# Kernel optimization log

Hardware: AMD Instinct MI355X
Metric: run time of the kernel (lower is better)

Reference implementation:

```python
import jax, jax.numpy as jnp
import numpy as np

B, C, F = 8, 2048, 128


def setup_inputs() -> dict:
    key = jax.random.key(0)
    ks = jax.random.split(key, 13)
    features = jax.random.normal(ks[0], (B, C, F), dtype=jnp.float32)
    # sparse-ish boolean adjacency masks over operations
    pred_mask = jax.random.uniform(ks[1], (B, C, C)) < 0.05
    succ_mask = jax.random.uniform(ks[2], (B, C, C)) < 0.05
    same_type_mask = jax.random.uniform(ks[3], (B, C, C)) < 0.10

    def linear(k, fan_in, fan_out):
        kw, kb = jax.random.split(k)
        bound = 1.0 / np.sqrt(fan_in)
        W = jax.random.uniform(kw, (fan_in, fan_out), minval=-bound, maxval=bound, dtype=jnp.float32)
        b = jax.random.uniform(kb, (fan_out,), minval=-bound, maxval=bound, dtype=jnp.float32)
        return W, b

    W_enc, b_enc = linear(ks[4], F, 4 * F)
    W_space, b_space = linear(ks[5], 3 * F, F)
    W_same, b_same = linear(ks[6], 2 * F, F)
    W_mix, b_mix = linear(ks[7], 2 * F, F)
    return {
        "features": features,
        "pred_mask": pred_mask,
        "succ_mask": succ_mask,
        "same_type_mask": same_type_mask,
        "W_enc": W_enc, "b_enc": b_enc,
        "W_space": W_space, "b_space": b_space,
        "W_same": W_same, "b_same": b_same,
        "W_mix": W_mix, "b_mix": b_mix,
    }


def reference(features, pred_mask, succ_mask, same_type_mask,
              W_enc, b_enc, W_space, b_space, W_same, b_same, W_mix, b_mix):
    # encoder: [B,C,F] -> [B,C,4F], split into origin + 3 message features
    enc = features @ W_enc + b_enc
    origin, e_pred, e_succ, e_same = jnp.split(enc, 4, axis=-1)

    def masked_mean(mask, e):
        # original builds (B,C,C,F) broadcast product then sums over 'other';
        # mathematically this is mask @ e with a clamped-degree divisor.
        m = mask.astype(e.dtype)                         # [B,C,C]
        deg = jnp.maximum(m.sum(-1, keepdims=True), 1.0)  # [B,C,1]
        return jnp.einsum('bij,bjf->bif', m, e) / deg

    pred_f = masked_mean(pred_mask, e_pred)
    succ_f = masked_mean(succ_mask, e_succ)
    same_f = masked_mean(same_type_mask, e_same)

    space_mixed = jnp.concatenate([pred_f, origin, succ_f], axis=-1) @ W_space + b_space
    same_mixed = jnp.concatenate([origin, same_f], axis=-1) @ W_same + b_same
    return jnp.concatenate([space_mixed, same_mixed], axis=-1) @ W_mix + b_mix
```

## Files before the change

### kernel.cpp

```cpp
#include <hip/hip_runtime.h>
#include <stdint.h>

typedef unsigned int uint;
typedef unsigned short ushort;
typedef unsigned char uchar;
typedef __attribute__((ext_vector_type(8))) short bf16x8;
typedef __attribute__((ext_vector_type(4))) float f32x4;

__device__ __forceinline__ ushort f2bf(float f) {
  uint u = __builtin_bit_cast(uint, f);
  return (ushort)((u + 0x7FFFu + ((u >> 16) & 1u)) >> 16);
}

__global__ __launch_bounds__(256) void k_detect(
    const uint* __restrict__ mp, const uint* __restrict__ ms,
    const uint* __restrict__ mt, int* __restrict__ esz) {
  int bid = blockIdx.x;
  const uint* m = (bid < 64) ? mp : (bid < 128) ? ms : mt;
  uint v = m[(size_t)(bid & 63) * 65521 + threadIdx.x];
  if (!(v == 0u || v == 1u || v == 0x3F800000u)) atomicAnd(esz, 0);
}

__global__ __launch_bounds__(256) void k_fuse1(
    const float* __restrict__ Ws, const float* __restrict__ Wsame,
    const float* __restrict__ Wm, float* __restrict__ T1, float* __restrict__ T2) {
  int idx = blockIdx.x * 256 + threadIdx.x;
  if (idx >= 81920) return;
  int r = idx >> 7, n = idx & 127;
  float s = 0.f;
  if (r < 384) {
    for (int c = 0; c < 128; ++c) s += Ws[r * 128 + c] * Wm[c * 128 + n];
    T1[r * 128 + n] = s;
  } else {
    int rr = r - 384;
    for (int c = 0; c < 128; ++c) s += Wsame[rr * 128 + c] * Wm[(128 + c) * 128 + n];
    T2[rr * 128 + n] = s;
  }
}

__global__ __launch_bounds__(256) void k_fuse2(
    const float* __restrict__ We, const float* __restrict__ be,
    const float* __restrict__ bs, const float* __restrict__ bsame,
    const float* __restrict__ bm, const float* __restrict__ Wm,
    const float* __restrict__ T1, const float* __restrict__ T2,
    ushort* __restrict__ UT, float* __restrict__ cvec) {
  int idx = blockIdx.x * 256 + threadIdx.x;
  if (idx < 65536) {
    int y = idx >> 14, n = (idx >> 7) & 127, k = idx & 127;
    float s = 0.f;
    if (y == 0)
      for (int m = 0; m < 128; ++m)
        s += We[k * 512 + m] * (T1[(128 + m) * 128 + n] + T2[m * 128 + n]);
    else if (y == 1)
      for (int m = 0; m < 128; ++m) s += We[k * 512 + 128 + m] * T1[m * 128 + n];
    else if (y == 2)
      for (int m = 0; m < 128; ++m) s += We[k * 512 + 256 + m] * T1[(256 + m) * 128 + n];
    else
      for (int m = 0; m < 128; ++m) s += We[k * 512 + 384 + m] * T2[(128 + m) * 128 + n];
    UT[((size_t)y * 128 + n) * 128 + k] = f2bf(s);
  } else if (idx < 66048) {
    int cid = idx - 65536, cv = cid >> 7, n = cid & 127;
    float s = 0.f;
    if (cv == 0) {
      for (int m = 0; m < 128; ++m)
        s += be[m] * (T1[(128 + m) * 128 + n] + T2[m * 128 + n]);
      for (int c = 0; c < 128; ++c) s += bs[c] * Wm[c * 128 + n];
      for (int c = 0; c < 128; ++c) s += bsame[c] * Wm[(128 + c) * 128 + n];
      s += bm[n];
    } else if (cv == 1) {
      for (int m = 0; m < 128; ++m) s += be[128 + m] * T1[m * 128 + n];
    } else if (cv == 2) {
      for (int m = 0; m < 128; ++m) s += be[256 + m] * T1[(256 + m) * 128 + n];
    } else {
      for (int m = 0; m < 128; ++m) s += be[384 + m] * T2[(128 + m) * 128 + n];
    }
    cvec[cv * 128 + n] = s;
  }
}

__global__ __launch_bounds__(256) void k_enc(
    const float* __restrict__ feat, const ushort* __restrict__ UT,
    const float* __restrict__ cvec, float* __restrict__ out,
    ushort* __restrict__ eT0, ushort* __restrict__ eT1, ushort* __restrict__ eT2) {
  __shared__ ushort As[64 * 72];
  __shared__ ushort Bs[128 * 72];
  __shared__ ushort stage[8192];
  const int t = threadIdx.x;
  const int gm0 = blockIdx.x * 64;
  const int y = blockIdx.y;
  const int lane = t & 63, wave = t >> 6;
  const int m0w = (wave >> 1) * 32, n0w = (wave & 1) * 64;
  const int quad = lane >> 4, lr = lane & 15;
  const int am = t >> 2, aq = t & 3;
  const int bn = t >> 1, bh = t & 1;
  f32x4 acc[2][4] = {};
  for (int k0 = 0; k0 < 128; k0 += 64) {
    const float* asrc = feat + (size_t)(gm0 + am) * 128 + k0 + aq * 16;
    float4 f0 = *(const float4*)asrc;
    float4 f1 = *(const float4*)(asrc + 4);
    float4 f2 = *(const float4*)(asrc + 8);
    float4 f3 = *(const float4*)(asrc + 12);
    ushort h[16];
    h[0] = f2bf(f0.x); h[1] = f2bf(f0.y); h[2] = f2bf(f0.z); h[3] = f2bf(f0.w);
    h[4] = f2bf(f1.x); h[5] = f2bf(f1.y); h[6] = f2bf(f1.z); h[7] = f2bf(f1.w);
    h[8] = f2bf(f2.x); h[9] = f2bf(f2.y); h[10] = f2bf(f2.z); h[11] = f2bf(f2.w);
    h[12] = f2bf(f3.x); h[13] = f2bf(f3.y); h[14] = f2bf(f3.z); h[15] = f2bf(f3.w);
    const ushort* bsrc = UT + ((size_t)y * 128 + bn) * 128 + k0 + bh * 32;
    bf16x8 bv0 = *(const bf16x8*)bsrc;
    bf16x8 bv1 = *(const bf16x8*)(bsrc + 8);
    bf16x8 bv2 = *(const bf16x8*)(bsrc + 16);
    bf16x8 bv3 = *(const bf16x8*)(bsrc + 24);
    *(bf16x8*)&As[am * 72 + aq * 16] = *(bf16x8*)&h[0];
    *(bf16x8*)&As[am * 72 + aq * 16 + 8] = *(bf16x8*)&h[8];
    *(bf16x8*)&Bs[bn * 72 + bh * 32] = bv0;
    *(bf16x8*)&Bs[bn * 72 + bh * 32 + 8] = bv1;
    *(bf16x8*)&Bs[bn * 72 + bh * 32 + 16] = bv2;
    *(bf16x8*)&Bs[bn * 72 + bh * 32 + 24] = bv3;
    __syncthreads();
#pragma unroll
    for (int kc = 0; kc < 2; ++kc) {
      bf16x8 a[2], b[4];
#pragma unroll
      for (int i = 0; i < 2; ++i)
        a[i] = *(const bf16x8*)&As[(m0w + i * 16 + lr) * 72 + kc * 32 + quad * 8];
#pragma unroll
      for (int j = 0; j < 4; ++j)
        b[j] = *(const bf16x8*)&Bs[(n0w + j * 16 + lr) * 72 + kc * 32 + quad * 8];
#pragma unroll
      for (int i = 0; i < 2; ++i)
#pragma unroll
        for (int j = 0; j < 4; ++j)
          acc[i][j] = __builtin_amdgcn_mfma_f32_16x16x32_bf16(a[i], b[j], acc[i][j], 0, 0, 0);
    }
    __syncthreads();
  }
  if (y == 0) {
#pragma unroll
    for (int i = 0; i < 2; ++i)
#pragma unroll
      for (int j = 0; j < 4; ++j)
#pragma unroll
        for (int r = 0; r < 4; ++r) {
          int m = gm0 + m0w + i * 16 + quad * 4 + r;
          int n = n0w + j * 16 + lr;
          out[(size_t)m * 128 + n] = acc[i][j][r] + cvec[n];
        }
  } else {
#pragma unroll
    for (int i = 0; i < 2; ++i)
#pragma unroll
      for (int j = 0; j < 4; ++j)
#pragma unroll
        for (int r = 0; r < 4; ++r) {
          int rl = m0w + i * 16 + quad * 4 + r;
          int n = n0w + j * 16 + lr;
          int kc = rl >> 5, qd = (rl >> 3) & 3, e = rl & 7;
          stage[((((n >> 4) * 2 + kc) * 4 + qd) * 16 + (n & 15)) * 8 + e] =
              f2bf(acc[i][j][r]);
        }
    __syncthreads();
    ushort* eT = (y == 1) ? eT0 : (y == 2) ? eT1 : eT2;
    ushort* dst = eT + ((size_t)(gm0 >> 11) * 32 + ((gm0 >> 6) & 31)) * 8192 + t * 32;
    const ushort* src = stage + t * 32;
#pragma unroll
    for (int p = 0; p < 4; ++p)
      *(bf16x8*)(dst + p * 8) = *(const bf16x8*)(src + p * 8);
  }
}

__global__ __launch_bounds__(256, 3) void k_mm(
    const void* __restrict__ mp, const void* __restrict__ ms,
    const void* __restrict__ mt, const ushort* __restrict__ eT0,
    const ushort* __restrict__ eT1, const ushort* __restrict__ eT2,
    const float* __restrict__ cvec, float* __restrict__ out,
    const int* __restrict__ esz_p) {
  __shared__ uint degs[64];
  const int t = threadIdx.x;
  const int id = blockIdx.x;
  const int xcd = id & 7, q = id >> 3;
  const int mtile = q & 31, gg = xcd * 3 + (q >> 5);
  const int b = gg & 7, mid = gg >> 3;
  const void* mask = (mid == 0) ? mp : (mid == 1) ? ms : mt;
  const ushort* eT = (mid == 0) ? eT0 : (mid == 1) ? eT1 : eT2;
  const float* cm = cvec + (mid + 1) * 128;
  const bool is4 = (*esz_p != 0);
  if (t < 64) degs[t] = 0;
  __syncthreads();

  const int lane = t & 63, wave = t >> 6;
  const int m0w = (wave >> 1) * 32, n0w = (wave & 1) * 64;
  const int quad = lane >> 4, lr = lane & 15;
  const int jb = n0w >> 4;
  const size_t rowbase = (size_t)b * 2048 + mtile * 64;
  const size_t r0 = rowbase + m0w + lr;
  const size_t r1 = r0 + 16;
  const uint* A40 = (const uint*)mask + r0 * 2048 + quad * 8;
  const uint* A41 = (const uint*)mask + r1 * 2048 + quad * 8;
  const uchar* A10 = (const uchar*)mask + r0 * 2048 + quad * 8;
  const uchar* A11 = (const uchar*)mask + r1 * 2048 + quad * 8;
  const ushort* bbase = eT + (size_t)b * 32 * 8192 + quad * 128 + lr * 8;

  f32x4 acc[2][4] = {};
  uint4 pa[2][2][2];
  uint2 pa8[2][2];
  bf16x8 pb[2][4];
  int cnt0 = 0, cnt1 = 0;

#define LOAD_ITER(IT, BUF)                                                   \
  do {                                                                       \
    int it_ = (IT);                                                          \
    if (is4) {                                                               \
      const uint* p0_ = A40 + it_ * 32;                                      \
      const uint* p1_ = A41 + it_ * 32;                                      \
      pa[BUF][0][0] = *(const uint4*)p0_;                                    \
      pa[BUF][0][1] = *(const uint4*)(p0_ + 4);                              \
      pa[BUF][1][0] = *(const uint4*)p1_;                                    \
      pa[BUF][1][1] = *(const uint4*)(p1_ + 4);                              \
    } else {                                                                 \
      pa8[BUF][0] = *(const uint2*)(A10 + it_ * 32);                         \
      pa8[BUF][1] = *(const uint2*)(A11 + it_ * 32);                         \
    }                                                                        \
    const ushort* bp_ = bbase + (it_ >> 1) * 8192 + (it_ & 1) * 512;         \
    _Pragma("unroll")                                                        \
    for (int j_ = 0; j_ < 4; ++j_)                                           \
      pb[BUF][j_] = *(const bf16x8*)(bp_ + (jb + j_) * 1024);                \
  } while (0)

  LOAD_ITER(0, 0);
#pragma unroll 2
  for (int it = 0; it < 64; ++it) {
    const int cur = it & 1;
    if (it < 63) LOAD_ITER(it + 1, cur ^ 1);
    union { bf16x8 v; uint u[4]; } af[2];
    if (is4) {
#pragma unroll
      for (int i = 0; i < 2; ++i) {
        uint x[8] = {pa[cur][i][0].x, pa[cur][i][0].y, pa[cur][i][0].z,
                     pa[cur][i][0].w, pa[cur][i][1].x, pa[cur][i][1].y,
                     pa[cur][i][1].z, pa[cur][i][1].w};
        int c = 0;
#pragma unroll
        for (int p = 0; p < 4; ++p) {
          af[i].u[p] = (x[2 * p] ? 0x3F80u : 0u) | (x[2 * p + 1] ? 0x3F800000u : 0u);
          c += (x[2 * p] != 0u) + (x[2 * p + 1] != 0u);
        }
        if (i == 0) cnt0 += c; else cnt1 += c;
      }
    } else {
#pragma unroll
      for (int i = 0; i < 2; ++i) {
        uint wl = pa8[cur][i].x, wh = pa8[cur][i].y;
        int c = 0;
        af[i].u[0] = ((wl & 0xFFu) ? 0x3F80u : 0u) | ((wl & 0xFF00u) ? 0x3F800000u : 0u);
        af[i].u[1] = ((wl & 0xFF0000u) ? 0x3F80u : 0u) | ((wl & 0xFF000000u) ? 0x3F800000u : 0u);
        af[i].u[2] = ((wh & 0xFFu) ? 0x3F80u : 0u) | ((wh & 0xFF00u) ? 0x3F800000u : 0u);
        af[i].u[3] = ((wh & 0xFF0000u) ? 0x3F80u : 0u) | ((wh & 0xFF000000u) ? 0x3F800000u : 0u);
        c += ((wl & 0xFFu) != 0u) + ((wl & 0xFF00u) != 0u) +
             ((wl & 0xFF0000u) != 0u) + ((wl & 0xFF000000u) != 0u) +
             ((wh & 0xFFu) != 0u) + ((wh & 0xFF00u) != 0u) +
             ((wh & 0xFF0000u) != 0u) + ((wh & 0xFF000000u) != 0u);
        if (i == 0) cnt0 += c; else cnt1 += c;
      }
    }
#pragma unroll
    for (int i = 0; i < 2; ++i)
#pragma unroll
      for (int j = 0; j < 4; ++j)
        acc[i][j] = __builtin_amdgcn_mfma_f32_16x16x32_bf16(af[i].v, pb[cur][j], acc[i][j], 0, 0, 0);
  }
#undef LOAD_ITER

  if ((wave & 1) == 0) {
    atomicAdd(&degs[m0w + lr], (uint)cnt0);
    atomicAdd(&degs[m0w + 16 + lr], (uint)cnt1);
  }
  __syncthreads();

#pragma unroll
  for (int i = 0; i < 2; ++i)
#pragma unroll
    for (int r = 0; r < 4; ++r) {
      int ml = m0w + i * 16 + quad * 4 + r;
      uint d = degs[ml];
      float inv = 1.0f / (float)(d > 0u ? d : 1u);
      float ind = (d > 0u) ? 1.0f : 0.0f;
#pragma unroll
      for (int j = 0; j < 4; ++j) {
        int n = n0w + j * 16 + lr;
        atomicAdd(&out[(rowbase + ml) * 128 + n], acc[i][j][r] * inv + ind * cm[n]);
      }
    }
}

extern "C" void kernel_launch(void* const* d_in, const int* in_sizes, int n_in,
                              void* d_out, int out_size, void* d_ws,
                              size_t ws_size, hipStream_t stream) {
  const float* features = (const float*)d_in[0];
  const void* pred = d_in[1];
  const void* succ = d_in[2];
  const void* same = d_in[3];
  const float* W_enc = (const float*)d_in[4];
  const float* b_enc = (const float*)d_in[5];
  const float* W_space = (const float*)d_in[6];
  const float* b_space = (const float*)d_in[7];
  const float* W_same = (const float*)d_in[8];
  const float* b_same = (const float*)d_in[9];
  const float* W_mix = (const float*)d_in[10];
  const float* b_mix = (const float*)d_in[11];
  float* out = (float*)d_out;

  char* wsb = (char*)d_ws;
  ushort* UT = (ushort*)wsb;
  float* cvec = (float*)(wsb + 131072);
  float* T1 = (float*)(wsb + 133120);
  float* T2 = (float*)(wsb + 329728);
  ushort* eT0 = (ushort*)(wsb + 460800);
  ushort* eT1 = (ushort*)(wsb + 460800 + 4194304);
  ushort* eT2 = (ushort*)(wsb + 460800 + 8388608);
  int* esz = (int*)(wsb + 460800 + 12582912);

  hipMemsetAsync(esz, 1, 4, stream);
  k_detect<<<192, 256, 0, stream>>>((const uint*)pred, (const uint*)succ,
                                    (const uint*)same, esz);
  k_fuse1<<<320, 256, 0, stream>>>(W_space, W_same, W_mix, T1, T2);
  k_fuse2<<<258, 256, 0, stream>>>(W_enc, b_enc, b_space, b_same, b_mix, W_mix,
                                   T1, T2, UT, cvec);
  k_enc<<<dim3(256, 4), 256, 0, stream>>>(features, UT, cvec, out, eT0, eT1, eT2);
  k_mm<<<768, 256, 0, stream>>>(pred, succ, same, eT0, eT1, eT2, cvec, out, esz);
}
```

Measured before the change: 470.3 us.

## Replace output atomics with per-mask partial buffers and a reduction kernel

The mask-matmul kernel now writes its per-mask results into three separate partial buffers instead of atomically adding into the output, and a new kernel sums them into the output. The k-index permutation of the mask and encoded-feature layout is changed so each lane loads contiguous 16-byte mask chunks. The main loop is restructured with explicit two-stage register prefetch for the 4-byte mask path, while the byte-mask path drops prefetching. This removes global float atomics at the cost of extra partial-buffer traffic and one more launch.

```diff
diff --git a/kernel.cpp b/kernel.cpp
--- a/kernel.cpp
+++ b/kernel.cpp
@@ -41,7 +41,7 @@
 __global__ __launch_bounds__(256) void k_fuse2(
     const float* __restrict__ We, const float* __restrict__ be,
     const float* __restrict__ bs, const float* __restrict__ bsame,
-    const float* __restrict__ bm, const float* __restrict__ Wm,
+    const float* __restrict__ bm_, const float* __restrict__ Wm,
     const float* __restrict__ T1, const float* __restrict__ T2,
     ushort* __restrict__ UT, float* __restrict__ cvec) {
   int idx = blockIdx.x * 256 + threadIdx.x;
@@ -66,7 +66,7 @@
         s += be[m] * (T1[(128 + m) * 128 + n] + T2[m * 128 + n]);
       for (int c = 0; c < 128; ++c) s += bs[c] * Wm[c * 128 + n];
       for (int c = 0; c < 128; ++c) s += bsame[c] * Wm[(128 + c) * 128 + n];
-      s += bm[n];
+      s += bm_[n];
     } else if (cv == 1) {
       for (int m = 0; m < 128; ++m) s += be[128 + m] * T1[m * 128 + n];
     } else if (cv == 2) {
@@ -152,9 +152,10 @@
       for (int j = 0; j < 4; ++j)
 #pragma unroll
         for (int r = 0; r < 4; ++r) {
-          int rl = m0w + i * 16 + quad * 4 + r;
+          int cl = m0w + i * 16 + quad * 4 + r;
+          int u = (cl & 32) + (((cl >> 2) & 3) * 8) + ((cl >> 4) & 1) * 4 + (cl & 3);
           int n = n0w + j * 16 + lr;
-          int kc = rl >> 5, qd = (rl >> 3) & 3, e = rl & 7;
+          int kc = u >> 5, qd = (u >> 3) & 3, e = u & 7;
           stage[((((n >> 4) * 2 + kc) * 4 + qd) * 16 + (n & 15)) * 8 + e] =
               f2bf(acc[i][j][r]);
         }
@@ -172,7 +173,8 @@
     const void* __restrict__ mp, const void* __restrict__ ms,
     const void* __restrict__ mt, const ushort* __restrict__ eT0,
     const ushort* __restrict__ eT1, const ushort* __restrict__ eT2,
-    const float* __restrict__ cvec, float* __restrict__ out,
+    const float* __restrict__ cvec, float* __restrict__ P0,
+    float* __restrict__ P1, float* __restrict__ P2,
     const int* __restrict__ esz_p) {
   __shared__ uint degs[64];
   const int t = threadIdx.x;
@@ -182,6 +184,7 @@
   const int b = gg & 7, mid = gg >> 3;
   const void* mask = (mid == 0) ? mp : (mid == 1) ? ms : mt;
   const ushort* eT = (mid == 0) ? eT0 : (mid == 1) ? eT1 : eT2;
+  float* Pm = (mid == 0) ? P0 : (mid == 1) ? P1 : P2;
   const float* cm = cvec + (mid + 1) * 128;
   const bool is4 = (*esz_p != 0);
   if (t < 64) degs[t] = 0;
@@ -194,81 +197,104 @@
   const size_t rowbase = (size_t)b * 2048 + mtile * 64;
   const size_t r0 = rowbase + m0w + lr;
   const size_t r1 = r0 + 16;
-  const uint* A40 = (const uint*)mask + r0 * 2048 + quad * 8;
-  const uint* A41 = (const uint*)mask + r1 * 2048 + quad * 8;
-  const uchar* A10 = (const uchar*)mask + r0 * 2048 + quad * 8;
-  const uchar* A11 = (const uchar*)mask + r1 * 2048 + quad * 8;
   const ushort* bbase = eT + (size_t)b * 32 * 8192 + quad * 128 + lr * 8;
 
   f32x4 acc[2][4] = {};
-  uint4 pa[2][2][2];
-  uint2 pa8[2][2];
-  bf16x8 pb[2][4];
   int cnt0 = 0, cnt1 = 0;
 
-#define LOAD_ITER(IT, BUF)                                                   \
-  do {                                                                       \
-    int it_ = (IT);                                                          \
-    if (is4) {                                                               \
-      const uint* p0_ = A40 + it_ * 32;                                      \
-      const uint* p1_ = A41 + it_ * 32;                                      \
-      pa[BUF][0][0] = *(const uint4*)p0_;                                    \
-      pa[BUF][0][1] = *(const uint4*)(p0_ + 4);                              \
-      pa[BUF][1][0] = *(const uint4*)p1_;                                    \
-      pa[BUF][1][1] = *(const uint4*)(p1_ + 4);                              \
-    } else {                                                                 \
-      pa8[BUF][0] = *(const uint2*)(A10 + it_ * 32);                         \
-      pa8[BUF][1] = *(const uint2*)(A11 + it_ * 32);                         \
-    }                                                                        \
-    const ushort* bp_ = bbase + (it_ >> 1) * 8192 + (it_ & 1) * 512;         \
-    _Pragma("unroll")                                                        \
-    for (int j_ = 0; j_ < 4; ++j_)                                           \
-      pb[BUF][j_] = *(const bf16x8*)(bp_ + (jb + j_) * 1024);                \
+  if (is4) {
+    const uint* A0b = (const uint*)mask + r0 * 2048 + quad * 4;
+    const uint* A1b = (const uint*)mask + r1 * 2048 + quad * 4;
+    uint4 p00, p01, p10, p11;
+    uint4 q00, q01, q10, q11;
+    bf16x8 pB[4], qB[4];
+
+#define MM_LOAD4(IT, A00, A01, A10, A11, PB)                                  \
+  do {                                                                        \
+    int it_ = (IT);                                                           \
+    if (it_ > 63) it_ = 63;                                                   \
+    const uint* p0_ = A0b + it_ * 32;                                         \
+    const uint* p1_ = A1b + it_ * 32;                                         \
+    A00 = *(const uint4*)p0_;                                                 \
+    A01 = *(const uint4*)(p0_ + 16);                                          \
+    A10 = *(const uint4*)p1_;                                                 \
+    A11 = *(const uint4*)(p1_ + 16);                                          \
+    const ushort* bp_ = bbase + (it_ >> 1) * 8192 + (it_ & 1) * 512;          \
+    _Pragma("unroll")                                                         \
+    for (int j_ = 0; j_ < 4; ++j_)                                            \
+      PB[j_] = *(const bf16x8*)(bp_ + (jb + j_) * 1024);                      \
   } while (0)
 
-  LOAD_ITER(0, 0);
-#pragma unroll 2
-  for (int it = 0; it < 64; ++it) {
-    const int cur = it & 1;
-    if (it < 63) LOAD_ITER(it + 1, cur ^ 1);
-    union { bf16x8 v; uint u[4]; } af[2];
-    if (is4) {
-#pragma unroll
-      for (int i = 0; i < 2; ++i) {
-        uint x[8] = {pa[cur][i][0].x, pa[cur][i][0].y, pa[cur][i][0].z,
-                     pa[cur][i][0].w, pa[cur][i][1].x, pa[cur][i][1].y,
-                     pa[cur][i][1].z, pa[cur][i][1].w};
-        int c = 0;
-#pragma unroll
-        for (int p = 0; p < 4; ++p) {
-          af[i].u[p] = (x[2 * p] ? 0x3F80u : 0u) | (x[2 * p + 1] ? 0x3F800000u : 0u);
-          c += (x[2 * p] != 0u) + (x[2 * p + 1] != 0u);
-        }
-        if (i == 0) cnt0 += c; else cnt1 += c;
+#define MM_STEP4(A00, A01, A10, A11, PB)                                      \
+  do {                                                                        \
+    union { bf16x8 v; uint u[4]; } af0, af1;                                  \
+    af0.u[0] = (A00.x ? 0x3F80u : 0u) | (A00.y ? 0x3F800000u : 0u);           \
+    af0.u[1] = (A00.z ? 0x3F80u : 0u) | (A00.w ? 0x3F800000u : 0u);           \
+    af0.u[2] = (A01.x ? 0x3F80u : 0u) | (A01.y ? 0x3F800000u : 0u);           \
+    af0.u[3] = (A01.z ? 0x3F80u : 0u) | (A01.w ? 0x3F800000u : 0u);           \
+    cnt0 += (A00.x != 0u) + (A00.y != 0u) + (A00.z != 0u) + (A00.w != 0u) +   \
+            (A01.x != 0u) + (A01.y != 0u) + (A01.z != 0u) + (A01.w != 0u);    \
+    af1.u[0] = (A10.x ? 0x3F80u : 0u) | (A10.y ? 0x3F800000u : 0u);           \
+    af1.u[1] = (A10.z ? 0x3F80u : 0u) | (A10.w ? 0x3F800000u : 0u);           \
+    af1.u[2] = (A11.x ? 0x3F80u : 0u) | (A11.y ? 0x3F800000u : 0u);           \
+    af1.u[3] = (A11.z ? 0x3F80u : 0u) | (A11.w ? 0x3F800000u : 0u);           \
+    cnt1 += (A10.x != 0u) + (A10.y != 0u) + (A10.z != 0u) + (A10.w != 0u) +   \
+            (A11.x != 0u) + (A11.y != 0u) + (A11.z != 0u) + (A11.w != 0u);    \
+    _Pragma("unroll")                                                         \
+    for (int j_ = 0; j_ < 4; ++j_) {                                          \
+      acc[0][j_] = __builtin_amdgcn_mfma_f32_16x16x32_bf16(af0.v, PB[j_],     \
+                                                           acc[0][j_], 0, 0, 0);\
+      acc[1][j_] = __builtin_amdgcn_mfma_f32_16x16x32_bf16(af1.v, PB[j_],     \
+                                                           acc[1][j_], 0, 0, 0);\
+    }                                                                         \
+  } while (0)
+
+    MM_LOAD4(0, p00, p01, p10, p11, pB);
+    MM_LOAD4(1, q00, q01, q10, q11, qB);
+    for (int it2 = 0; it2 < 32; ++it2) {
+      MM_STEP4(p00, p01, p10, p11, pB);
+      MM_LOAD4(2 * it2 + 2, p00, p01, p10, p11, pB);
+      MM_STEP4(q00, q01, q10, q11, qB);
+      MM_LOAD4(2 * it2 + 3, q00, q01, q10, q11, qB);
+    }
+#undef MM_LOAD4
+#undef MM_STEP4
+  } else {
+    const uchar* B0b = (const uchar*)mask + r0 * 2048 + quad * 4;
+    const uchar* B1b = (const uchar*)mask + r1 * 2048 + quad * 4;
+    for (int it = 0; it < 64; ++it) {
+      uint lo0 = *(const uint*)(B0b + it * 32);
+      uint hi0 = *(const uint*)(B0b + it * 32 + 16);
+      uint lo1 = *(const uint*)(B1b + it * 32);
+      uint hi1 = *(const uint*)(B1b + it * 32 + 16);
+      bf16x8 pb[4];
+      const ushort* bp = bbase + (it >> 1) * 8192 + (it & 1) * 512;
+#pragma unroll
+      for (int j = 0; j < 4; ++j) pb[j] = *(const bf16x8*)(bp + (jb + j) * 1024);
+      union { bf16x8 v; uint u[4]; } af0, af1;
+      af0.u[0] = ((lo0 & 0xFFu) ? 0x3F80u : 0u) | ((lo0 & 0xFF00u) ? 0x3F800000u : 0u);
+      af0.u[1] = ((lo0 & 0xFF0000u) ? 0x3F80u : 0u) | ((lo0 & 0xFF000000u) ? 0x3F800000u : 0u);
+      af0.u[2] = ((hi0 & 0xFFu) ? 0x3F80u : 0u) | ((hi0 & 0xFF00u) ? 0x3F800000u : 0u);
+      af0.u[3] = ((hi0 & 0xFF0000u) ? 0x3F80u : 0u) | ((hi0 & 0xFF000000u) ? 0x3F800000u : 0u);
+      af1.u[0] = ((lo1 & 0xFFu) ? 0x3F80u : 0u) | ((lo1 & 0xFF00u) ? 0x3F800000u : 0u);
+      af1.u[1] = ((lo1 & 0xFF0000u) ? 0x3F80u : 0u) | ((lo1 & 0xFF000000u) ? 0x3F800000u : 0u);
+      af1.u[2] = ((hi1 & 0xFFu) ? 0x3F80u : 0u) | ((hi1 & 0xFF00u) ? 0x3F800000u : 0u);
+      af1.u[3] = ((hi1 & 0xFF0000u) ? 0x3F80u : 0u) | ((hi1 & 0xFF000000u) ? 0x3F800000u : 0u);
+      cnt0 += ((lo0 & 0xFFu) != 0u) + ((lo0 & 0xFF00u) != 0u) +
+              ((lo0 & 0xFF0000u) != 0u) + ((lo0 & 0xFF000000u) != 0u) +
+              ((hi0 & 0xFFu) != 0u) + ((hi0 & 0xFF00u) != 0u) +
+              ((hi0 & 0xFF0000u) != 0u) + ((hi0 & 0xFF000000u) != 0u);
+      cnt1 += ((lo1 & 0xFFu) != 0u) + ((lo1 & 0xFF00u) != 0u) +
+              ((lo1 & 0xFF0000u) != 0u) + ((lo1 & 0xFF000000u) != 0u) +
+              ((hi1 & 0xFFu) != 0u) + ((hi1 & 0xFF00u) != 0u) +
+              ((hi1 & 0xFF0000u) != 0u) + ((hi1 & 0xFF000000u) != 0u);
+#pragma unroll
+      for (int j = 0; j < 4; ++j) {
+        acc[0][j] = __builtin_amdgcn_mfma_f32_16x16x32_bf16(af0.v, pb[j], acc[0][j], 0, 0, 0);
+        acc[1][j] = __builtin_amdgcn_mfma_f32_16x16x32_bf16(af1.v, pb[j], acc[1][j], 0, 0, 0);
       }
-    } else {
-#pragma unroll
-      for (int i = 0; i < 2; ++i) {
-        uint wl = pa8[cur][i].x, wh = pa8[cur][i].y;
-        int c = 0;
-        af[i].u[0] = ((wl & 0xFFu) ? 0x3F80u : 0u) | ((wl & 0xFF00u) ? 0x3F800000u : 0u);
-        af[i].u[1] = ((wl & 0xFF0000u) ? 0x3F80u : 0u) | ((wl & 0xFF000000u) ? 0x3F800000u : 0u);
-        af[i].u[2] = ((wh & 0xFFu) ? 0x3F80u : 0u) | ((wh & 0xFF00u) ? 0x3F800000u : 0u);
-        af[i].u[3] = ((wh & 0xFF0000u) ? 0x3F80u : 0u) | ((wh & 0xFF000000u) ? 0x3F800000u : 0u);
-        c += ((wl & 0xFFu) != 0u) + ((wl & 0xFF00u) != 0u) +
-             ((wl & 0xFF0000u) != 0u) + ((wl & 0xFF000000u) != 0u) +
-             ((wh & 0xFFu) != 0u) + ((wh & 0xFF00u) != 0u) +
-             ((wh & 0xFF0000u) != 0u) + ((wh & 0xFF000000u) != 0u);
-        if (i == 0) cnt0 += c; else cnt1 += c;
-      }
-    }
-#pragma unroll
-    for (int i = 0; i < 2; ++i)
-#pragma unroll
-      for (int j = 0; j < 4; ++j)
-        acc[i][j] = __builtin_amdgcn_mfma_f32_16x16x32_bf16(af[i].v, pb[cur][j], acc[i][j], 0, 0, 0);
-  }
-#undef LOAD_ITER
+    }
+  }
 
   if ((wave & 1) == 0) {
     atomicAdd(&degs[m0w + lr], (uint)cnt0);
@@ -276,20 +302,37 @@
   }
   __syncthreads();
 
+  float cmv[4];
+#pragma unroll
+  for (int j = 0; j < 4; ++j) cmv[j] = cm[n0w + j * 16 + lr];
 #pragma unroll
   for (int i = 0; i < 2; ++i)
 #pragma unroll
     for (int r = 0; r < 4; ++r) {
-      int ml = m0w + i * 16 + quad * 4 + r;
-      uint d = degs[ml];
-      float inv = 1.0f / (float)(d > 0u ? d : 1u);
-      float ind = (d > 0u) ? 1.0f : 0.0f;
+      const int ml = m0w + i * 16 + quad * 4 + r;
+      const size_t row = rowbase + ml;
+      const uint d = degs[ml];
+      const float iv = 1.0f / (float)(d > 0u ? d : 1u);
+      const float id_ = (d > 0u) ? 1.0f : 0.0f;
 #pragma unroll
       for (int j = 0; j < 4; ++j) {
-        int n = n0w + j * 16 + lr;
-        atomicAdd(&out[(rowbase + ml) * 128 + n], acc[i][j][r] * inv + ind * cm[n]);
+        const int n = n0w + j * 16 + lr;
+        Pm[row * 128 + n] = acc[i][j][r] * iv + id_ * cmv[j];
       }
     }
+}
+
+__global__ __launch_bounds__(256) void k_add(
+    float4* __restrict__ out, const float4* __restrict__ P0,
+    const float4* __restrict__ P1, const float4* __restrict__ P2) {
+  const int i = blockIdx.x * 256 + threadIdx.x;
+  float4 o = out[i];
+  const float4 a = P0[i], b = P1[i], c = P2[i];
+  o.x += a.x + b.x + c.x;
+  o.y += a.y + b.y + c.y;
+  o.z += a.z + b.z + c.z;
+  o.w += a.w + b.w + c.w;
+  out[i] = o;
 }
 
 extern "C" void kernel_launch(void* const* d_in, const int* in_sizes, int n_in,
@@ -317,7 +360,10 @@
   ushort* eT0 = (ushort*)(wsb + 460800);
   ushort* eT1 = (ushort*)(wsb + 460800 + 4194304);
   ushort* eT2 = (ushort*)(wsb + 460800 + 8388608);
-  int* esz = (int*)(wsb + 460800 + 12582912);
+  float* P0 = (float*)(wsb + 13043712);
+  float* P1 = (float*)(wsb + 13043712 + 8388608);
+  float* P2 = (float*)(wsb + 13043712 + 16777216);
+  int* esz = (int*)(wsb + 38209536);
 
   hipMemsetAsync(esz, 1, 4, stream);
   k_detect<<<192, 256, 0, stream>>>((const uint*)pred, (const uint*)succ,
@@ -326,5 +372,8 @@
   k_fuse2<<<258, 256, 0, stream>>>(W_enc, b_enc, b_space, b_same, b_mix, W_mix,
                                    T1, T2, UT, cvec);
   k_enc<<<dim3(256, 4), 256, 0, stream>>>(features, UT, cvec, out, eT0, eT1, eT2);
-  k_mm<<<768, 256, 0, stream>>>(pred, succ, same, eT0, eT1, eT2, cvec, out, esz);
-}
+  k_mm<<<768, 256, 0, stream>>>(pred, succ, same, eT0, eT1, eT2, cvec,
+                                P0, P1, P2, esz);
+  k_add<<<2048, 256, 0, stream>>>((float4*)out, (const float4*)P0,
+                                  (const float4*)P1, (const float4*)P2);
+}
```

Result: slower. 549.5 us (+16.8%).
